# Kernel optimization log

Hardware: AMD Instinct MI355X
Metric: run time of the kernel (lower is better)

## Reference

```python
import jax, jax.numpy as jnp
import numpy as np

B, T, F, C, L, W, NT, H = 4096, 64, 32, 64, 256, 512, 8, 12

# Tsit5 Butcher tableau (fixed-step, 6-stage FSAL-free form)
A21 = 0.161
A31, A32 = -0.008480655492356989, 0.335480655492357
A41, A42, A43 = 2.8971530571054935, -6.359448489975075, 4.362295432869581
A51, A52, A53, A54 = 5.325864828439257, -11.748883564062828, 7.4955393428898365, -0.09249506636175525
A61, A62, A63, A64, A65 = 5.86145544294642, -12.92096931784711, 8.159367898576159, -0.071584973281401, -0.028269050394068383
BC1, BC2, BC3, BC4, BC5, BC6 = 0.09646076681806523, 0.01, 0.4798896504144996, 1.379008574103742, -3.290069515436081, 2.324710524099774
SUBSTEPS = 10  # dt0 = 0.1, integrate each unit interval with 10 fixed steps


def setup_inputs() -> dict:
    key = jax.random.key(0)
    ks = jax.random.split(key, 16)
    def lin(k, out_d, in_d, scale=None):
        s = (1.0 / np.sqrt(in_d)) if scale is None else scale
        return jax.random.normal(k, (out_d, in_d), jnp.float32) * s
    inp = {
        "x_seq": jax.random.normal(ks[0], (B, T, F), jnp.float32),
        "country_idx": jax.random.randint(ks[1], (B,), 0, C),
        "horizon": H,
        # GRU encoder params (equinox GRUCell layout: 3*hidden stacked r,z,n)
        "W_ih": lin(ks[2], 3 * L, F + C),
        "W_hh": lin(ks[3], 3 * L, L),
        "b_ih": jnp.zeros((3 * L,), jnp.float32),
        "b_n": jnp.zeros((L,), jnp.float32),
        # NeuralField MLP 256->512->512->256, small init to keep the ODE stable
        "W0": lin(ks[4], W, L, 0.1 / np.sqrt(L)),
        "b0": jnp.zeros((W,), jnp.float32),
        "W1": lin(ks[5], W, W, 0.1 / np.sqrt(W)),
        "b1": jnp.zeros((W,), jnp.float32),
        "W2": lin(ks[6], L, W, 0.1 / np.sqrt(W)),
        "b2": jnp.zeros((L,), jnp.float32),
        # Decoder
        "W_dec": lin(ks[7], NT, L),
        "b_dec": jnp.zeros((NT,), jnp.float32),
    }
    return inp


def reference(x_seq, W_ih, W_hh, b_ih, b_n, W0, b0, W1, b1, W2, b2, W_dec, b_dec, country_idx, horizon):
    dtype = x_seq.dtype
    n_countries = W_ih.shape[1] - x_seq.shape[2]
    n_latent = W_hh.shape[1]
    ohe = jax.nn.one_hot(country_idx, n_countries, dtype=dtype)  # [B, C]

    # ---- GRU encoder scan over time ----
    h0 = jnp.zeros((x_seq.shape[0], n_latent), dtype)
    def gru_step(h, x_t):
        x_in = jnp.concatenate([x_t, ohe], axis=-1)          # [B, F+C]
        ih = x_in @ W_ih.T + b_ih                            # [B, 3L]
        hh = h @ W_hh.T                                      # [B, 3L]
        ir, iz, inn = jnp.split(ih, 3, axis=-1)
        hr, hz, hn = jnp.split(hh, 3, axis=-1)
        r = jax.nn.sigmoid(ir + hr)
        z = jax.nn.sigmoid(iz + hz)
        n = jnp.tanh(inn + r * (hn + b_n))
        return n + z * (h - n), None
    h_final, _ = jax.lax.scan(gru_step, h0, jnp.swapaxes(x_seq, 0, 1))

    # ---- Neural ODE vector field (autonomous ELU MLP) ----
    def f(y):
        a = jax.nn.elu(y @ W0.T + b0)
        a = jax.nn.elu(a @ W1.T + b1)
        return a @ W2.T + b2

    dt = jnp.asarray(1.0 / SUBSTEPS, dtype)
    def tsit5_step(y, _):
        k1 = f(y)
        k2 = f(y + dt * (A21 * k1))
        k3 = f(y + dt * (A31 * k1 + A32 * k2))
        k4 = f(y + dt * (A41 * k1 + A42 * k2 + A43 * k3))
        k5 = f(y + dt * (A51 * k1 + A52 * k2 + A53 * k3 + A54 * k4))
        k6 = f(y + dt * (A61 * k1 + A62 * k2 + A63 * k3 + A64 * k4 + A65 * k5))
        y_new = y + dt * (BC1 * k1 + BC2 * k2 + BC3 * k3 + BC4 * k4 + BC5 * k5 + BC6 * k6)
        return y_new, None

    def unit(y, _):
        y, _ = jax.lax.scan(tsit5_step, y, None, length=SUBSTEPS)
        return y, y  # save state at each integer time t = 1..horizon

    _, ys = jax.lax.scan(unit, h_final, None, length=horizon)  # [H, B, L]

    # ---- linear decode ----
    out = jnp.einsum('hbl,tl->bht', ys, W_dec) + b_dec  # [B, H, n_targets]
    return out
```

## Files before the change

### kernel.cpp

```cpp
#include <hip/hip_runtime.h>

typedef __bf16 bf16;
typedef __bf16 bf16x8 __attribute__((ext_vector_type(8)));
typedef float  f32x4  __attribute__((ext_vector_type(4)));

#define B_TOT 4096
#define T_SEQ 64
#define NT_OUT 8
#define NTHR 512
#define NBLK 256
#define GSZ  8

#define WS_W0   0
#define WS_W1   262144
#define WS_W2   786432
#define WS_WHH  1048576
#define WS_WIH  1441792
#define WS_BC   1490944
#define WS_GY   2097152
#define WS_GYB  4194304
#define WS_GH1  6291456
#define WS_GH2  10485760
#define WS_FLG  14680064
#define WS_MAP  14688256

constexpr float A21 = 0.161f;
constexpr float A31 = -0.008480655492356989f, A32 = 0.335480655492357f;
constexpr float A41 = 2.8971530571054935f, A42 = -6.359448489975075f, A43 = 4.362295432869581f;
constexpr float A51 = 5.325864828439257f, A52 = -11.748883564062828f, A53 = 7.4955393428898365f, A54 = -0.09249506636175525f;
constexpr float A61 = 5.86145544294642f, A62 = -12.92096931784711f, A63 = 8.159367898576159f, A64 = -0.071584973281401f, A65 = -0.028269050394068383f;
constexpr float BC1 = 0.09646076681806523f, BC2 = 0.01f, BC3 = 0.4798896504144996f;
constexpr float BC4 = 1.379008574103742f, BC5 = -3.290069515436081f, BC6 = 2.324710524099774f;
constexpr float DT = 0.1f;
constexpr float BROW[5][5] = {
    {A21, 0, 0, 0, 0},
    {A31, A32, 0, 0, 0},
    {A41, A42, A43, 0, 0},
    {A51, A52, A53, A54, 0},
    {A61, A62, A63, A64, A65}};
constexpr float FCF[6] = {BC1, BC2, BC3, BC4, BC5, BC6};

__device__ __forceinline__ f32x4 MFMA(bf16x8 a, bf16x8 b, f32x4 c) {
    return __builtin_amdgcn_mfma_f32_16x16x32_bf16(a, b, c, 0, 0, 0);
}
__device__ __forceinline__ float eluf(float x) { return x > 0.f ? x : __expf(x) - 1.f; }
__device__ __forceinline__ float sigm_f(float x) { return 1.f / (1.f + __expf(-x)); }
__device__ __forceinline__ float tanh_f(float x) { return 1.f - 2.f / (__expf(2.f * x) + 1.f); }

template<bool FAST>
__device__ __forceinline__ void ld4g(const bf16* p, bf16x8& a0, bf16x8& a1, bf16x8& a2, bf16x8& a3) {
    if constexpr (FAST) {
        asm volatile(
            "global_load_dwordx4 %0, %4, off sc0\n\t"
            "global_load_dwordx4 %1, %4, off offset:1024 sc0\n\t"
            "global_load_dwordx4 %2, %4, off offset:2048 sc0\n\t"
            "global_load_dwordx4 %3, %4, off offset:3072 sc0"
            : "=&v"(a0), "=&v"(a1), "=&v"(a2), "=&v"(a3)
            : "v"(p) : "memory");
    } else {
        asm volatile(
            "global_load_dwordx4 %0, %4, off sc0 sc1\n\t"
            "global_load_dwordx4 %1, %4, off offset:1024 sc0 sc1\n\t"
            "global_load_dwordx4 %2, %4, off offset:2048 sc0 sc1\n\t"
            "global_load_dwordx4 %3, %4, off offset:3072 sc0 sc1"
            : "=&v"(a0), "=&v"(a1), "=&v"(a2), "=&v"(a3)
            : "v"(p) : "memory");
    }
}
template<bool FAST>
__device__ __forceinline__ bf16x8 ld1g(const bf16* p) {
    bf16x8 a;
    if constexpr (FAST)
        asm volatile("global_load_dwordx4 %0, %1, off sc0\n\ts_waitcnt vmcnt(0)"
                     : "=v"(a) : "v"(p) : "memory");
    else
        asm volatile("global_load_dwordx4 %0, %1, off sc0 sc1\n\ts_waitcnt vmcnt(0)"
                     : "=v"(a) : "v"(p) : "memory");
    return a;
}
template<bool FAST>
__device__ __forceinline__ void st8g(bf16* p, bf16x8 v) {
    if constexpr (FAST) *(bf16x8*)p = v;
    else asm volatile("global_store_dwordx4 %0, %1, off sc0 sc1" :: "v"(p), "v"(v) : "memory");
}
__device__ __forceinline__ void vmwait() {
    asm volatile("s_waitcnt vmcnt(0)" ::: "memory");
    __builtin_amdgcn_sched_barrier(0);
}

__device__ __forceinline__ void produce(unsigned* f, int tid) {
    asm volatile("s_waitcnt vmcnt(0)" ::: "memory");
    __syncthreads();
    if (tid == 0) __hip_atomic_fetch_add(f, 1u, __ATOMIC_RELAXED, __HIP_MEMORY_SCOPE_AGENT);
}
__device__ __forceinline__ void consume(unsigned* f, unsigned tgt, int tid) {
    if (tid == 0) {
        while (__hip_atomic_load(f, __ATOMIC_RELAXED, __HIP_MEMORY_SCOPE_AGENT) < tgt)
            __builtin_amdgcn_s_sleep(8);
    }
    __syncthreads();
}

template<bool FAST>
__device__ __forceinline__ void decode(const bf16* gY, const float* sWdec, const float* sBdec,
                                       float* bncF, float* __restrict__ out,
                                       int tid, int g, int j, int H, int u) {
    {
        const int row = tid >> 5, seg = tid & 31;
        bf16x8 yv = ld1g<FAST>(gY + ((j * 8 + (seg >> 2)) * 64 + row + (seg & 3) * 16) * 8);
        #pragma unroll
        for (int e = 0; e < 8; ++e) bncF[row * 256 + seg * 8 + e] = (float)yv[e];
    }
    __syncthreads();
    if (tid < 128) {
        const int row = tid >> 3, tt = tid & 7;
        float acc = sBdec[tt];
        const float* wd = sWdec + tt * 256;
        const float* yr = bncF + row * 256;
        #pragma unroll 8
        for (int i = 0; i < 256; i += 4) {
            f32x4 yv = *(const f32x4*)&yr[i];
            acc += yv[0] * wd[i] + yv[1] * wd[i + 1] + yv[2] * wd[i + 2] + yv[3] * wd[i + 3];
        }
        out[((size_t)(g * 128 + 16 * j + row) * H + u) * NT_OUT + tt] = acc;
    }
    __syncthreads();
}

template<int ST, bool FAST>
__device__ __forceinline__ void ode_stage(
    const bf16* sW0, const bf16* sW1, const bf16* sW2, bf16* bnc,
    bf16* gY, bf16* gH1, bf16* gH2,
    unsigned* fY, unsigned* fH1, unsigned* fH2,
    const float (&b0r)[4], const float (&b1r)[4], const float (&b2r)[2],
    f32x4 (&yreg)[2], f32x4 (&kreg)[5][2],
    int tid, int m, int lane, int j,
    unsigned& eY, unsigned& eH1, unsigned& eH2) {
    const int lm = lane & 15, q4 = (lane >> 4) << 2;
    const f32x4 Z = {0.f, 0.f, 0.f, 0.f};

    {
        bf16x8 a[8];
        const bf16* pA = gY + m * 4096 + lane * 8;
        ld4g<FAST>(pA, a[0], a[1], a[2], a[3]);
        ld4g<FAST>(pA + 2048, a[4], a[5], a[6], a[7]);
        vmwait();
        f32x4 acc[4] = {Z, Z, Z, Z};
        #pragma unroll
        for (int kk = 0; kk < 8; ++kk)
            #pragma unroll
            for (int nt = 0; nt < 4; ++nt)
                acc[nt] = MFMA(a[kk], *(const bf16x8*)&sW0[(nt * 8 + kk) * 512 + lane * 8], acc[nt]);
        #pragma unroll
        for (int nt = 0; nt < 4; ++nt) {
            const int oct = 2 * (nt & 1) + (lm >> 3);
            const int base = (m * 2 + (nt >> 1)) * 512;
            #pragma unroll
            for (int r = 0; r < 4; ++r)
                bnc[base + ((q4 + r) + oct * 16) * 8 + (lm & 7)] = (bf16)eluf(acc[nt][r] + b0r[nt]);
        }
    }
    __syncthreads();
    {
        const int i = tid * 16, mm = i >> 10, rem = i & 1023;
        bf16* d = gH1 + mm * 8192 + (2 * j + (rem >> 9)) * 512 + (rem & 511);
        st8g<FAST>(d, *(const bf16x8*)&bnc[i]);
        st8g<FAST>(d + 8, *(const bf16x8*)&bnc[i + 8]);
    }
    produce(fH1, tid); ++eH1;
    consume(fH1, GSZ * eH1, tid);

    {
        bf16x8 a[16];
        const bf16* pA = gH1 + m * 8192 + lane * 8;
        ld4g<FAST>(pA, a[0], a[1], a[2], a[3]);
        ld4g<FAST>(pA + 2048, a[4], a[5], a[6], a[7]);
        ld4g<FAST>(pA + 4096, a[8], a[9], a[10], a[11]);
        ld4g<FAST>(pA + 6144, a[12], a[13], a[14], a[15]);
        vmwait();
        f32x4 acc[4] = {Z, Z, Z, Z};
        #pragma unroll
        for (int kk = 0; kk < 16; ++kk)
            #pragma unroll
            for (int nt = 0; nt < 4; ++nt)
                acc[nt] = MFMA(a[kk], *(const bf16x8*)&sW1[(nt * 16 + kk) * 512 + lane * 8], acc[nt]);
        #pragma unroll
        for (int nt = 0; nt < 4; ++nt) {
            const int oct = 2 * (nt & 1) + (lm >> 3);
            const int base = (m * 2 + (nt >> 1)) * 512;
            #pragma unroll
            for (int r = 0; r < 4; ++r)
                bnc[base + ((q4 + r) + oct * 16) * 8 + (lm & 7)] = (bf16)eluf(acc[nt][r] + b1r[nt]);
        }
    }
    __syncthreads();
    {
        const int i = tid * 16, mm = i >> 10, rem = i & 1023;
        bf16* d = gH2 + mm * 8192 + (2 * j + (rem >> 9)) * 512 + (rem & 511);
        st8g<FAST>(d, *(const bf16x8*)&bnc[i]);
        st8g<FAST>(d + 8, *(const bf16x8*)&bnc[i + 8]);
    }
    produce(fH2, tid); ++eH2;
    consume(fH2, GSZ * eH2, tid);

    {
        bf16x8 a[16];
        const bf16* pA = gH2 + m * 8192 + lane * 8;
        ld4g<FAST>(pA, a[0], a[1], a[2], a[3]);
        ld4g<FAST>(pA + 2048, a[4], a[5], a[6], a[7]);
        ld4g<FAST>(pA + 4096, a[8], a[9], a[10], a[11]);
        ld4g<FAST>(pA + 6144, a[12], a[13], a[14], a[15]);
        vmwait();
        f32x4 kk2[2] = {Z, Z};
        #pragma unroll
        for (int kk = 0; kk < 16; ++kk)
            #pragma unroll
            for (int nt = 0; nt < 2; ++nt)
                kk2[nt] = MFMA(a[kk], *(const bf16x8*)&sW2[(nt * 16 + kk) * 512 + lane * 8], kk2[nt]);
        #pragma unroll
        for (int nt = 0; nt < 2; ++nt)
            #pragma unroll
            for (int r = 0; r < 4; ++r) kk2[nt][r] += b2r[nt];

        f32x4 yst[2];
        if constexpr (ST < 5) {
            kreg[ST][0] = kk2[0]; kreg[ST][1] = kk2[1];
            #pragma unroll
            for (int nt = 0; nt < 2; ++nt) {
                yst[nt] = yreg[nt];
                #pragma unroll
                for (int i = 0; i <= ST; ++i) {
                    const float c = DT * BROW[ST][i];
                    #pragma unroll
                    for (int r = 0; r < 4; ++r) yst[nt][r] += c * kreg[i][nt][r];
                }
            }
        } else {
            #pragma unroll
            for (int nt = 0; nt < 2; ++nt) {
                #pragma unroll
                for (int i = 0; i < 5; ++i) {
                    const float c = DT * FCF[i];
                    #pragma unroll
                    for (int r = 0; r < 4; ++r) yreg[nt][r] += c * kreg[i][nt][r];
                }
                #pragma unroll
                for (int r = 0; r < 4; ++r) yreg[nt][r] += (DT * FCF[5]) * kk2[nt][r];
                yst[nt] = yreg[nt];
            }
        }
        #pragma unroll
        for (int nt = 0; nt < 2; ++nt) {
            const int oct = 2 * nt + (lm >> 3);
            #pragma unroll
            for (int r = 0; r < 4; ++r)
                bnc[(m * 64 + (q4 + r) + oct * 16) * 8 + (lm & 7)] = (bf16)yst[nt][r];
        }
    }
    __syncthreads();
    {
        const int i = tid * 8, mm = i >> 9, rem = i & 511;
        st8g<FAST>(gY + mm * 4096 + j * 512 + rem, *(const bf16x8*)&bnc[i]);
    }
    produce(fY, tid); ++eY;
}

template<bool FAST>
__device__ void body(const float* __restrict__ x_seq, const int* __restrict__ cidx,
                     const float* __restrict__ b_n, const float* __restrict__ b0,
                     const float* __restrict__ b1, const float* __restrict__ b2,
                     const float* __restrict__ W_dec, const float* __restrict__ b_dec,
                     char* __restrict__ ws, float* __restrict__ out, char* SM,
                     int H, int g, int j) {
    const int tid = threadIdx.x, m = tid >> 6, lane = tid & 63;
    const int lm = lane & 15, q = lane >> 4, q4 = q << 2;
    const int grow0 = g * 128;

    const bf16* W0p  = (const bf16*)(ws + WS_W0);
    const bf16* W1p  = (const bf16*)(ws + WS_W1);
    const bf16* W2p  = (const bf16*)(ws + WS_W2);
    const bf16* WhhP = (const bf16*)(ws + WS_WHH);
    const bf16* WihP = (const bf16*)(ws + WS_WIH);
    const float* bias_c = (const float*)(ws + WS_BC);
    bf16* gY  = (bf16*)(ws + WS_GY)  + (size_t)g * 32768;
    bf16* gYb = (bf16*)(ws + WS_GYB) + (size_t)g * 32768;
    bf16* gH1 = (bf16*)(ws + WS_GH1) + (size_t)g * 65536;
    bf16* gH2 = (bf16*)(ws + WS_GH2) + (size_t)g * 65536;
    unsigned* fl = (unsigned*)(ws + WS_FLG) + (size_t)g * 64;
    unsigned *fY = fl, *fH1 = fl + 16, *fH2 = fl + 32;

    bf16*  sWgt  = (bf16*)SM;
    bf16*  bnc   = (bf16*)(SM + 131072);
    float* bncF  = (float*)(SM + 131072);
    float* sWdec = (float*)(SM + 147456);
    float* sBdec = (float*)(SM + 155648);

    unsigned eY = 0, eH1 = 0, eH2 = 0;

    for (int i = tid; i < 2048; i += NTHR) sWdec[i] = W_dec[i];
    if (tid < 8) sBdec[tid] = b_dec[tid];

    bf16* sGhh = sWgt;
    bf16* sGih = sWgt + 24576;
    for (int i = tid; i < 3072; i += NTHR) {
        const int gh = i >> 9, inner = (i & 511) << 3;
        const int c = (gh >> 1) * 16 + 2 * j + (gh & 1);
        *(bf16x8*)&sGhh[gh * 4096 + inner] = *(const bf16x8*)&WhhP[(size_t)c * 4096 + inner];
    }
    for (int i = tid; i < 384; i += NTHR) {
        const int gh = i >> 6, inner = (i & 63) << 3;
        const int c = (gh >> 1) * 16 + 2 * j + (gh & 1);
        *(bf16x8*)&sGih[gh * 512 + inner] = *(const bf16x8*)&WihP[(size_t)c * 512 + inner];
    }

    float bcr[2][4], bcz[2][4], bcn[2][4], bnr[2];
    #pragma unroll
    for (int h = 0; h < 2; ++h) {
        const int F = 32 * j + 16 * h + lm;
        bnr[h] = b_n[F];
        #pragma unroll
        for (int r = 0; r < 4; ++r) {
            const int c = cidx[grow0 + 16 * m + q4 + r];
            bcr[h][r] = bias_c[(size_t)c * 768 + F];
            bcz[h][r] = bias_c[(size_t)c * 768 + 256 + F];
            bcn[h][r] = bias_c[(size_t)c * 768 + 512 + F];
        }
    }
    __syncthreads();

    {
        bf16x8 zz;
        #pragma unroll
        for (int e = 0; e < 8; ++e) zz[e] = (bf16)0.f;
        const int i = tid * 8, mm = i >> 9, rem = i & 511;
        st8g<FAST>(gY + mm * 4096 + j * 512 + rem, zz);
    }
    produce(fY, tid); ++eY;

    f32x4 hreg[2] = {{0.f,0.f,0.f,0.f},{0.f,0.f,0.f,0.f}};
    const f32x4 Z = {0.f, 0.f, 0.f, 0.f};

    for (int t = 0; t < T_SEQ; ++t) {
        consume(fY, GSZ * eY, tid);
        const bf16* hb = (t & 1) ? gYb : gY;
        bf16x8 a[8];
        const bf16* pA = hb + m * 4096 + lane * 8;
        ld4g<FAST>(pA, a[0], a[1], a[2], a[3]);
        ld4g<FAST>(pA + 2048, a[4], a[5], a[6], a[7]);
        bf16x8 ax;
        {
            const float* xp = x_seq + (((size_t)(grow0 + 16 * m + lm)) * T_SEQ + t) * 32 + 8 * q;
            f32x4 xa = *(const f32x4*)xp;
            f32x4 xb = *(const f32x4*)(xp + 4);
            #pragma unroll
            for (int e = 0; e < 4; ++e) { ax[e] = (bf16)xa[e]; ax[4 + e] = (bf16)xb[e]; }
        }
        vmwait();
        f32x4 aRZ[4] = {Z, Z, Z, Z}, aNH[2] = {Z, Z}, aNX[2] = {Z, Z};
        #pragma unroll
        for (int kk = 0; kk < 8; ++kk) {
            #pragma unroll
            for (int h = 0; h < 2; ++h) {
                aRZ[h]     = MFMA(a[kk], *(const bf16x8*)&sGhh[(0 + h) * 4096 + kk * 512 + lane * 8], aRZ[h]);
                aRZ[2 + h] = MFMA(a[kk], *(const bf16x8*)&sGhh[(2 + h) * 4096 + kk * 512 + lane * 8], aRZ[2 + h]);
                aNH[h]     = MFMA(a[kk], *(const bf16x8*)&sGhh[(4 + h) * 4096 + kk * 512 + lane * 8], aNH[h]);
            }
        }
        #pragma unroll
        for (int h = 0; h < 2; ++h) {
            aRZ[h]     = MFMA(ax, *(const bf16x8*)&sGih[(0 + h) * 512 + lane * 8], aRZ[h]);
            aRZ[2 + h] = MFMA(ax, *(const bf16x8*)&sGih[(2 + h) * 512 + lane * 8], aRZ[2 + h]);
            aNX[h]     = MFMA(ax, *(const bf16x8*)&sGih[(4 + h) * 512 + lane * 8], aNX[h]);
        }
        #pragma unroll
        for (int h = 0; h < 2; ++h) {
            const int oct = 2 * h + (lm >> 3);
            #pragma unroll
            for (int r = 0; r < 4; ++r) {
                const float rg = sigm_f(aRZ[h][r] + bcr[h][r]);
                const float zg = sigm_f(aRZ[2 + h][r] + bcz[h][r]);
                const float nn = tanh_f(aNX[h][r] + bcn[h][r] + rg * (aNH[h][r] + bnr[h]));
                const float hp = nn + zg * (hreg[h][r] - nn);
                hreg[h][r] = hp;
                bnc[(m * 64 + (q4 + r) + oct * 16) * 8 + (lm & 7)] = (bf16)hp;
            }
        }
        __syncthreads();
        {
            bf16* wb = ((t + 1) & 1) ? gYb : gY;
            const int i = tid * 8, mm = i >> 9, rem = i & 511;
            st8g<FAST>(wb + mm * 4096 + j * 512 + rem, *(const bf16x8*)&bnc[i]);
        }
        produce(fY, tid); ++eY;
    }

    bf16* sW0 = sWgt;
    bf16* sW1 = sWgt + 16384;
    bf16* sW2 = sWgt + 49152;
    for (int i = tid; i < 2048; i += NTHR)
        *(bf16x8*)&sW0[i * 8] = *(const bf16x8*)&W0p[(size_t)j * 16384 + i * 8];
    for (int i = tid; i < 4096; i += NTHR)
        *(bf16x8*)&sW1[i * 8] = *(const bf16x8*)&W1p[(size_t)j * 32768 + i * 8];
    for (int i = tid; i < 2048; i += NTHR)
        *(bf16x8*)&sW2[i * 8] = *(const bf16x8*)&W2p[(size_t)j * 16384 + i * 8];

    float b0r[4], b1r[4], b2r[2];
    #pragma unroll
    for (int nt = 0; nt < 4; ++nt) {
        b0r[nt] = b0[64 * j + nt * 16 + lm];
        b1r[nt] = b1[64 * j + nt * 16 + lm];
    }
    #pragma unroll
    for (int nt = 0; nt < 2; ++nt) b2r[nt] = b2[32 * j + nt * 16 + lm];
    __syncthreads();

    f32x4 yreg[2] = {hreg[0], hreg[1]};
    f32x4 kreg[5][2];

    const int NSS = H * 10;
    for (int ss = 0; ss < NSS; ++ss) {
        consume(fY, GSZ * eY, tid);
        if (ss && (ss % 10) == 0)
            decode<FAST>(gY, sWdec, sBdec, bncF, out, tid, g, j, H, ss / 10 - 1);
        ode_stage<0, FAST>(sW0, sW1, sW2, bnc, gY, gH1, gH2, fY, fH1, fH2, b0r, b1r, b2r, yreg, kreg, tid, m, lane, j, eY, eH1, eH2);
        consume(fY, GSZ * eY, tid);
        ode_stage<1, FAST>(sW0, sW1, sW2, bnc, gY, gH1, gH2, fY, fH1, fH2, b0r, b1r, b2r, yreg, kreg, tid, m, lane, j, eY, eH1, eH2);
        consume(fY, GSZ * eY, tid);
        ode_stage<2, FAST>(sW0, sW1, sW2, bnc, gY, gH1, gH2, fY, fH1, fH2, b0r, b1r, b2r, yreg, kreg, tid, m, lane, j, eY, eH1, eH2);
        consume(fY, GSZ * eY, tid);
        ode_stage<3, FAST>(sW0, sW1, sW2, bnc, gY, gH1, gH2, fY, fH1, fH2, b0r, b1r, b2r, yreg, kreg, tid, m, lane, j, eY, eH1, eH2);
        consume(fY, GSZ * eY, tid);
        ode_stage<4, FAST>(sW0, sW1, sW2, bnc, gY, gH1, gH2, fY, fH1, fH2, b0r, b1r, b2r, yreg, kreg, tid, m, lane, j, eY, eH1, eH2);
        consume(fY, GSZ * eY, tid);
        ode_stage<5, FAST>(sW0, sW1, sW2, bnc, gY, gH1, gH2, fY, fH1, fH2, b0r, b1r, b2r, yreg, kreg, tid, m, lane, j, eY, eH1, eH2);
    }
    consume(fY, GSZ * eY, tid);
    decode<FAST>(gY, sWdec, sBdec, bncF, out, tid, g, j, H, H - 1);
}

__global__ void __launch_bounds__(NTHR, 2)
k_main(const float* __restrict__ x_seq, const int* __restrict__ cidx,
       const float* __restrict__ b_n, const float* __restrict__ b0,
       const float* __restrict__ b1, const float* __restrict__ b2,
       const float* __restrict__ W_dec, const float* __restrict__ b_dec,
       char* __restrict__ ws, float* __restrict__ out, int H) {
    __shared__ __align__(16) char SM[155712];
    const int tid = threadIdx.x, b = blockIdx.x;
    const int x8 = b & 7, rr = b >> 3, mg = rr >> 3, j = rr & 7;
    const int g = x8 * 4 + mg;

    unsigned* xmap = (unsigned*)(ws + WS_MAP);
    unsigned* gctr = (unsigned*)(ws + WS_MAP + 1024);
    unsigned xcc;
    asm volatile("s_getreg_b32 %0, hwreg(HW_REG_XCC_ID)" : "=s"(xcc));
    if (tid == 0) {
        __hip_atomic_store(&xmap[b], xcc, __ATOMIC_RELAXED, __HIP_MEMORY_SCOPE_AGENT);
        __hip_atomic_fetch_add(gctr, 1u, __ATOMIC_RELAXED, __HIP_MEMORY_SCOPE_AGENT);
        while (__hip_atomic_load(gctr, __ATOMIC_RELAXED, __HIP_MEMORY_SCOPE_AGENT) < NBLK)
            __builtin_amdgcn_s_sleep(8);
    }
    __syncthreads();
    unsigned* mapL = (unsigned*)(SM + 131072);
    if (tid < NBLK)
        mapL[tid] = __hip_atomic_load(&xmap[tid], __ATOMIC_RELAXED, __HIP_MEMORY_SCOPE_AGENT);
    __syncthreads();
    int* fastP = (int*)(SM + 155696);
    if (tid == 0) {
        const unsigned my = mapL[b];
        int cnt = 0;
        for (int i = 0; i < NBLK; ++i) cnt += (mapL[i] == my) ? 1 : 0;
        int ok = (cnt == 32) ? 1 : 0;
        for (int i = 0; i < GSZ; ++i) ok &= (mapL[x8 + 8 * (mg * 8 + i)] == my) ? 1 : 0;
        *fastP = ok;
    }
    __syncthreads();
    const int fastf = *fastP;
    __syncthreads();

    if (fastf)
        body<true>(x_seq, cidx, b_n, b0, b1, b2, W_dec, b_dec, ws, out, (char*)SM, H, g, j);
    else
        body<false>(x_seq, cidx, b_n, b0, b1, b2, W_dec, b_dec, ws, out, (char*)SM, H, g, j);
}

__global__ void k_pack(const float* __restrict__ src, bf16* __restrict__ dst,
                       int OUT, int K, int Ksrc, int koff) {
    const int total = (OUT * K) >> 3;
    for (int gg = blockIdx.x * blockDim.x + threadIdx.x; gg < total; gg += gridDim.x * blockDim.x) {
        const int lane = gg & 63, f = gg >> 6;
        const int KK = K >> 5;
        const int kk = f % KK, c = f / KK;
        const int col = c * 16 + (lane & 15);
        const int k0 = kk * 32 + ((lane >> 4) << 3);
        bf16x8 o;
        #pragma unroll
        for (int jj = 0; jj < 8; ++jj) o[jj] = (bf16)src[(size_t)col * Ksrc + koff + k0 + jj];
        *(bf16x8*)&dst[(size_t)gg * 8] = o;
    }
}

__global__ void k_bias(const float* __restrict__ W_ih, const float* __restrict__ b_ih,
                       float* __restrict__ bias_c) {
    const int i = blockIdx.x * blockDim.x + threadIdx.x;
    if (i < 64 * 768) {
        const int c = i / 768, n = i - c * 768;
        bias_c[i] = W_ih[(size_t)n * 96 + 32 + c] + b_ih[n];
    }
}

extern "C" void kernel_launch(void* const* d_in, const int* in_sizes, int n_in,
                              void* d_out, int out_size, void* d_ws, size_t ws_size,
                              hipStream_t stream) {
    const float* x_seq = (const float*)d_in[0];
    const int*   cidx  = (const int*)d_in[1];
    const float* W_ih  = (const float*)d_in[3];
    const float* W_hh  = (const float*)d_in[4];
    const float* b_ih  = (const float*)d_in[5];
    const float* b_n   = (const float*)d_in[6];
    const float* W0    = (const float*)d_in[7];
    const float* b0    = (const float*)d_in[8];
    const float* W1    = (const float*)d_in[9];
    const float* b1    = (const float*)d_in[10];
    const float* W2    = (const float*)d_in[11];
    const float* b2    = (const float*)d_in[12];
    const float* W_dec = (const float*)d_in[13];
    const float* b_dec = (const float*)d_in[14];
    float* out = (float*)d_out;
    const int H = out_size / (B_TOT * NT_OUT);
    char* ws = (char*)d_ws;

    hipMemsetAsync(ws + WS_FLG, 0, 16384, stream);

    k_pack<<<64, 256, 0, stream>>>(W0, (bf16*)(ws + WS_W0), 512, 256, 256, 0);
    k_pack<<<128, 256, 0, stream>>>(W1, (bf16*)(ws + WS_W1), 512, 512, 512, 0);
    k_pack<<<64, 256, 0, stream>>>(W2, (bf16*)(ws + WS_W2), 256, 512, 512, 0);
    k_pack<<<96, 256, 0, stream>>>(W_hh, (bf16*)(ws + WS_WHH), 768, 256, 256, 0);
    k_pack<<<12, 256, 0, stream>>>(W_ih, (bf16*)(ws + WS_WIH), 768, 32, 96, 0);
    k_bias<<<(64 * 768 + 255) / 256, 256, 0, stream>>>(W_ih, b_ih, (float*)(ws + WS_BC));

    k_main<<<NBLK, NTHR, 0, stream>>>(x_seq, cidx, b_n, b0, b1, b2, W_dec, b_dec,
                                      ws, out, H);
}
```

Baseline: 6.731 ms.

## Swap MFMA operands to write outputs directly to global, drop LDS staging

Reorganizes the per-wave GEMM mapping so weights become the A operand and activations the B operand. Each lane can then write its bf16 results straight to the global exchange buffers in the consumer's layout, which removes the LDS bounce buffer and the extra __syncthreads before each store. The decoder is rewritten as a warp-shuffle reduction without LDS staging, GRU weights are interleaved into a single LDS array, and the spin-wait sleep is shortened. The trade-off is smaller, less coalesced 8-byte global stores and changed work partitioning across waves.

```diff
diff --git a/kernel.cpp b/kernel.cpp
--- a/kernel.cpp
+++ b/kernel.cpp
@@ -2,7 +2,9 @@
 
 typedef __bf16 bf16;
 typedef __bf16 bf16x8 __attribute__((ext_vector_type(8)));
+typedef __bf16 bf16x4 __attribute__((ext_vector_type(4)));
 typedef float  f32x4  __attribute__((ext_vector_type(4)));
+typedef unsigned int u32;
 
 #define B_TOT 4096
 #define T_SEQ 64
@@ -17,12 +19,12 @@
 #define WS_WHH  1048576
 #define WS_WIH  1441792
 #define WS_BC   1490944
-#define WS_GY   2097152
-#define WS_GYB  4194304
-#define WS_GH1  6291456
-#define WS_GH2  10485760
-#define WS_FLG  14680064
-#define WS_MAP  14688256
+#define WS_GY   1703936
+#define WS_GYB  3801088
+#define WS_GH1  5898240
+#define WS_GH2  10092544
+#define WS_FLG  14286848
+#define WS_MAP  14290944
 
 constexpr float A21 = 0.161f;
 constexpr float A31 = -0.008480655492356989f, A32 = 0.335480655492357f;
@@ -55,16 +57,14 @@
             "global_load_dwordx4 %1, %4, off offset:1024 sc0\n\t"
             "global_load_dwordx4 %2, %4, off offset:2048 sc0\n\t"
             "global_load_dwordx4 %3, %4, off offset:3072 sc0"
-            : "=&v"(a0), "=&v"(a1), "=&v"(a2), "=&v"(a3)
-            : "v"(p) : "memory");
+            : "=&v"(a0), "=&v"(a1), "=&v"(a2), "=&v"(a3) : "v"(p) : "memory");
     } else {
         asm volatile(
             "global_load_dwordx4 %0, %4, off sc0 sc1\n\t"
             "global_load_dwordx4 %1, %4, off offset:1024 sc0 sc1\n\t"
             "global_load_dwordx4 %2, %4, off offset:2048 sc0 sc1\n\t"
             "global_load_dwordx4 %3, %4, off offset:3072 sc0 sc1"
-            : "=&v"(a0), "=&v"(a1), "=&v"(a2), "=&v"(a3)
-            : "v"(p) : "memory");
+            : "=&v"(a0), "=&v"(a1), "=&v"(a2), "=&v"(a3) : "v"(p) : "memory");
     }
 }
 template<bool FAST>
@@ -79,190 +79,154 @@
     return a;
 }
 template<bool FAST>
-__device__ __forceinline__ void st8g(bf16* p, bf16x8 v) {
-    if constexpr (FAST) *(bf16x8*)p = v;
-    else asm volatile("global_store_dwordx4 %0, %1, off sc0 sc1" :: "v"(p), "v"(v) : "memory");
+__device__ __forceinline__ void st4g(bf16* p, bf16x4 v) {
+    if constexpr (FAST) *(bf16x4*)p = v;
+    else asm volatile("global_store_dwordx2 %0, %1, off sc0 sc1" :: "v"(p), "v"(v) : "memory");
 }
 __device__ __forceinline__ void vmwait() {
     asm volatile("s_waitcnt vmcnt(0)" ::: "memory");
     __builtin_amdgcn_sched_barrier(0);
 }
 
-__device__ __forceinline__ void produce(unsigned* f, int tid) {
+__device__ __forceinline__ void produce(u32* f, int tid) {
     asm volatile("s_waitcnt vmcnt(0)" ::: "memory");
     __syncthreads();
     if (tid == 0) __hip_atomic_fetch_add(f, 1u, __ATOMIC_RELAXED, __HIP_MEMORY_SCOPE_AGENT);
 }
-__device__ __forceinline__ void consume(unsigned* f, unsigned tgt, int tid) {
+__device__ __forceinline__ void consume(const u32* f, u32 tgt, int tid) {
     if (tid == 0) {
         while (__hip_atomic_load(f, __ATOMIC_RELAXED, __HIP_MEMORY_SCOPE_AGENT) < tgt)
-            __builtin_amdgcn_s_sleep(8);
-    }
-    __syncthreads();
-}
-
-template<bool FAST>
-__device__ __forceinline__ void decode(const bf16* gY, const float* sWdec, const float* sBdec,
-                                       float* bncF, float* __restrict__ out,
-                                       int tid, int g, int j, int H, int u) {
-    {
-        const int row = tid >> 5, seg = tid & 31;
-        bf16x8 yv = ld1g<FAST>(gY + ((j * 8 + (seg >> 2)) * 64 + row + (seg & 3) * 16) * 8);
-        #pragma unroll
-        for (int e = 0; e < 8; ++e) bncF[row * 256 + seg * 8 + e] = (float)yv[e];
-    }
-    __syncthreads();
-    if (tid < 128) {
-        const int row = tid >> 3, tt = tid & 7;
-        float acc = sBdec[tt];
-        const float* wd = sWdec + tt * 256;
-        const float* yr = bncF + row * 256;
-        #pragma unroll 8
-        for (int i = 0; i < 256; i += 4) {
-            f32x4 yv = *(const f32x4*)&yr[i];
-            acc += yv[0] * wd[i] + yv[1] * wd[i + 1] + yv[2] * wd[i + 2] + yv[3] * wd[i + 3];
-        }
-        out[((size_t)(g * 128 + 16 * j + row) * H + u) * NT_OUT + tt] = acc;
-    }
-    __syncthreads();
+            __builtin_amdgcn_s_sleep(1);
+    }
+    __syncthreads();
+}
+
+template<int KK, int NM, bool FAST>
+__device__ __forceinline__ void gemm_core(const bf16* sWl, const bf16* ginl, int MSIN,
+                                          f32x4 (&acc)[NM]) {
+    bf16x8 wr[KK];
+    #pragma unroll
+    for (int kk = 0; kk < KK; ++kk) wr[kk] = *(const bf16x8*)&sWl[kk * 512];
+    #pragma unroll
+    for (int m = 0; m < NM; ++m) {
+        bf16x8 a[KK];
+        const bf16* p = ginl + m * MSIN;
+        #pragma unroll
+        for (int kq = 0; kq < KK; kq += 4)
+            ld4g<FAST>(p + kq * 512, a[kq], a[kq + 1], a[kq + 2], a[kq + 3]);
+        vmwait();
+        f32x4 e = {0.f, 0.f, 0.f, 0.f}, o = {0.f, 0.f, 0.f, 0.f};
+        #pragma unroll
+        for (int kk = 0; kk < KK; kk += 2) {
+            e = MFMA(wr[kk], a[kk], e);
+            o = MFMA(wr[kk + 1], a[kk + 1], o);
+        }
+        acc[m] = e + o;
+    }
+}
+
+template<bool ELU, int NM, bool FAST>
+__device__ __forceinline__ void store_out(bf16* dst, int MS, const float (&bias)[4],
+                                          const f32x4 (&acc)[NM]) {
+    #pragma unroll
+    for (int m = 0; m < NM; ++m) {
+        bf16x4 ov;
+        #pragma unroll
+        for (int r = 0; r < 4; ++r) {
+            float v = acc[m][r] + bias[r];
+            if constexpr (ELU) v = eluf(v);
+            ov[r] = (bf16)v;
+        }
+        st4g<FAST>(dst + m * MS, ov);
+    }
 }
 
 template<int ST, bool FAST>
 __device__ __forceinline__ void ode_stage(
-    const bf16* sW0, const bf16* sW1, const bf16* sW2, bf16* bnc,
-    bf16* gY, bf16* gH1, bf16* gH2,
-    unsigned* fY, unsigned* fH1, unsigned* fH2,
-    const float (&b0r)[4], const float (&b1r)[4], const float (&b2r)[2],
+    const bf16* sW0l, const bf16* sW1l, const bf16* sW2l,
+    const bf16* gYl, bf16* gH1d, const bf16* gH1l, bf16* gH2d, const bf16* gH2l, bf16* gYd,
+    u32* fY, u32* fH1, u32* fH2, int tid,
+    const float (&b0w)[4], const float (&b1w)[4], const float (&b2w)[4],
     f32x4 (&yreg)[2], f32x4 (&kreg)[5][2],
-    int tid, int m, int lane, int j,
-    unsigned& eY, unsigned& eH1, unsigned& eH2) {
-    const int lm = lane & 15, q4 = (lane >> 4) << 2;
-    const f32x4 Z = {0.f, 0.f, 0.f, 0.f};
-
+    u32& eY, u32& eH1, u32& eH2) {
     {
-        bf16x8 a[8];
-        const bf16* pA = gY + m * 4096 + lane * 8;
-        ld4g<FAST>(pA, a[0], a[1], a[2], a[3]);
-        ld4g<FAST>(pA + 2048, a[4], a[5], a[6], a[7]);
-        vmwait();
-        f32x4 acc[4] = {Z, Z, Z, Z};
-        #pragma unroll
-        for (int kk = 0; kk < 8; ++kk)
-            #pragma unroll
-            for (int nt = 0; nt < 4; ++nt)
-                acc[nt] = MFMA(a[kk], *(const bf16x8*)&sW0[(nt * 8 + kk) * 512 + lane * 8], acc[nt]);
-        #pragma unroll
-        for (int nt = 0; nt < 4; ++nt) {
-            const int oct = 2 * (nt & 1) + (lm >> 3);
-            const int base = (m * 2 + (nt >> 1)) * 512;
-            #pragma unroll
-            for (int r = 0; r < 4; ++r)
-                bnc[base + ((q4 + r) + oct * 16) * 8 + (lm & 7)] = (bf16)eluf(acc[nt][r] + b0r[nt]);
-        }
-    }
-    __syncthreads();
-    {
-        const int i = tid * 16, mm = i >> 10, rem = i & 1023;
-        bf16* d = gH1 + mm * 8192 + (2 * j + (rem >> 9)) * 512 + (rem & 511);
-        st8g<FAST>(d, *(const bf16x8*)&bnc[i]);
-        st8g<FAST>(d + 8, *(const bf16x8*)&bnc[i + 8]);
+        f32x4 acc[4];
+        gemm_core<8, 4, FAST>(sW0l, gYl, 4096, acc);
+        store_out<true, 4, FAST>(gH1d, 8192, b0w, acc);
     }
     produce(fH1, tid); ++eH1;
     consume(fH1, GSZ * eH1, tid);
-
     {
-        bf16x8 a[16];
-        const bf16* pA = gH1 + m * 8192 + lane * 8;
-        ld4g<FAST>(pA, a[0], a[1], a[2], a[3]);
-        ld4g<FAST>(pA + 2048, a[4], a[5], a[6], a[7]);
-        ld4g<FAST>(pA + 4096, a[8], a[9], a[10], a[11]);
-        ld4g<FAST>(pA + 6144, a[12], a[13], a[14], a[15]);
-        vmwait();
-        f32x4 acc[4] = {Z, Z, Z, Z};
-        #pragma unroll
-        for (int kk = 0; kk < 16; ++kk)
-            #pragma unroll
-            for (int nt = 0; nt < 4; ++nt)
-                acc[nt] = MFMA(a[kk], *(const bf16x8*)&sW1[(nt * 16 + kk) * 512 + lane * 8], acc[nt]);
-        #pragma unroll
-        for (int nt = 0; nt < 4; ++nt) {
-            const int oct = 2 * (nt & 1) + (lm >> 3);
-            const int base = (m * 2 + (nt >> 1)) * 512;
-            #pragma unroll
-            for (int r = 0; r < 4; ++r)
-                bnc[base + ((q4 + r) + oct * 16) * 8 + (lm & 7)] = (bf16)eluf(acc[nt][r] + b1r[nt]);
-        }
-    }
-    __syncthreads();
-    {
-        const int i = tid * 16, mm = i >> 10, rem = i & 1023;
-        bf16* d = gH2 + mm * 8192 + (2 * j + (rem >> 9)) * 512 + (rem & 511);
-        st8g<FAST>(d, *(const bf16x8*)&bnc[i]);
-        st8g<FAST>(d + 8, *(const bf16x8*)&bnc[i + 8]);
+        f32x4 acc[4];
+        gemm_core<16, 4, FAST>(sW1l, gH1l, 8192, acc);
+        store_out<true, 4, FAST>(gH2d, 8192, b1w, acc);
     }
     produce(fH2, tid); ++eH2;
     consume(fH2, GSZ * eH2, tid);
-
     {
-        bf16x8 a[16];
-        const bf16* pA = gH2 + m * 8192 + lane * 8;
-        ld4g<FAST>(pA, a[0], a[1], a[2], a[3]);
-        ld4g<FAST>(pA + 2048, a[4], a[5], a[6], a[7]);
-        ld4g<FAST>(pA + 4096, a[8], a[9], a[10], a[11]);
-        ld4g<FAST>(pA + 6144, a[12], a[13], a[14], a[15]);
-        vmwait();
-        f32x4 kk2[2] = {Z, Z};
-        #pragma unroll
-        for (int kk = 0; kk < 16; ++kk)
+        f32x4 acc[2];
+        gemm_core<16, 2, FAST>(sW2l, gH2l, 8192, acc);
+        #pragma unroll
+        for (int i = 0; i < 2; ++i) {
+            f32x4 kv;
             #pragma unroll
-            for (int nt = 0; nt < 2; ++nt)
-                kk2[nt] = MFMA(a[kk], *(const bf16x8*)&sW2[(nt * 16 + kk) * 512 + lane * 8], kk2[nt]);
-        #pragma unroll
-        for (int nt = 0; nt < 2; ++nt)
-            #pragma unroll
-            for (int r = 0; r < 4; ++r) kk2[nt][r] += b2r[nt];
-
-        f32x4 yst[2];
-        if constexpr (ST < 5) {
-            kreg[ST][0] = kk2[0]; kreg[ST][1] = kk2[1];
-            #pragma unroll
-            for (int nt = 0; nt < 2; ++nt) {
-                yst[nt] = yreg[nt];
+            for (int r = 0; r < 4; ++r) kv[r] = acc[i][r] + b2w[r];
+            f32x4 yst;
+            if constexpr (ST < 5) {
+                kreg[ST][i] = kv;
+                yst = yreg[i];
                 #pragma unroll
-                for (int i = 0; i <= ST; ++i) {
-                    const float c = DT * BROW[ST][i];
+                for (int s = 0; s <= ST; ++s) {
+                    const float c = DT * BROW[ST][s];
                     #pragma unroll
-                    for (int r = 0; r < 4; ++r) yst[nt][r] += c * kreg[i][nt][r];
+                    for (int r = 0; r < 4; ++r) yst[r] += c * kreg[s][i][r];
                 }
-            }
-        } else {
-            #pragma unroll
-            for (int nt = 0; nt < 2; ++nt) {
+            } else {
                 #pragma unroll
-                for (int i = 0; i < 5; ++i) {
-                    const float c = DT * FCF[i];
+                for (int s = 0; s < 5; ++s) {
+                    const float c = DT * FCF[s];
                     #pragma unroll
-                    for (int r = 0; r < 4; ++r) yreg[nt][r] += c * kreg[i][nt][r];
+                    for (int r = 0; r < 4; ++r) yreg[i][r] += c * kreg[s][i][r];
                 }
                 #pragma unroll
-                for (int r = 0; r < 4; ++r) yreg[nt][r] += (DT * FCF[5]) * kk2[nt][r];
-                yst[nt] = yreg[nt];
+                for (int r = 0; r < 4; ++r) yreg[i][r] += (DT * FCF[5]) * kv[r];
+                yst = yreg[i];
             }
-        }
-        #pragma unroll
-        for (int nt = 0; nt < 2; ++nt) {
-            const int oct = 2 * nt + (lm >> 3);
+            bf16x4 ov;
             #pragma unroll
-            for (int r = 0; r < 4; ++r)
-                bnc[(m * 64 + (q4 + r) + oct * 16) * 8 + (lm & 7)] = (bf16)yst[nt][r];
-        }
-    }
-    __syncthreads();
-    {
-        const int i = tid * 8, mm = i >> 9, rem = i & 511;
-        st8g<FAST>(gY + mm * 4096 + j * 512 + rem, *(const bf16x8*)&bnc[i]);
+            for (int r = 0; r < 4; ++r) ov[r] = (bf16)yst[r];
+            st4g<FAST>(gYd + i * 4096, ov);
+        }
     }
     produce(fY, tid); ++eY;
+}
+
+template<bool FAST>
+__device__ __forceinline__ void dec_unit(const bf16* gY, const float* sWdec, const float* sBdec,
+                                         float* out, int g, int j, int w, int lane, int H, int u) {
+    const int rloc = 2 * w + (lane >> 5);
+    const int li = lane & 31;
+    const bf16* p = gY + (size_t)j * 4096 + (((li >> 2) * 64 + (li & 3) * 16 + rloc)) * 8;
+    bf16x8 yv = ld1g<FAST>(p);
+    const int f0 = li * 8;
+    float acc[8];
+    #pragma unroll
+    for (int t = 0; t < 8; ++t) acc[t] = 0.f;
+    #pragma unroll
+    for (int e = 0; e < 8; ++e) {
+        const float yf = (float)yv[e];
+        #pragma unroll
+        for (int t = 0; t < 8; ++t) acc[t] += yf * sWdec[t * 256 + f0 + e];
+    }
+    #pragma unroll
+    for (int k = 1; k < 32; k <<= 1)
+        #pragma unroll
+        for (int t = 0; t < 8; ++t) acc[t] += __shfl_xor(acc[t], k, 64);
+    if (li == 0) {
+        const size_t row = (size_t)g * 128 + 16 * j + rloc;
+        #pragma unroll
+        for (int t = 0; t < 8; ++t) out[(row * H + u) * NT_OUT + t] = acc[t] + sBdec[t];
+    }
 }
 
 template<bool FAST>
@@ -272,7 +236,7 @@
                      const float* __restrict__ W_dec, const float* __restrict__ b_dec,
                      char* __restrict__ ws, float* __restrict__ out, char* SM,
                      int H, int g, int j) {
-    const int tid = threadIdx.x, m = tid >> 6, lane = tid & 63;
+    const int tid = threadIdx.x, w = tid >> 6, lane = tid & 63;
     const int lm = lane & 15, q = lane >> 4, q4 = q << 2;
     const int grow0 = g * 128;
 
@@ -286,110 +250,103 @@
     bf16* gYb = (bf16*)(ws + WS_GYB) + (size_t)g * 32768;
     bf16* gH1 = (bf16*)(ws + WS_GH1) + (size_t)g * 65536;
     bf16* gH2 = (bf16*)(ws + WS_GH2) + (size_t)g * 65536;
-    unsigned* fl = (unsigned*)(ws + WS_FLG) + (size_t)g * 64;
-    unsigned *fY = fl, *fH1 = fl + 16, *fH2 = fl + 32;
+    u32* fl  = (u32*)(ws + WS_FLG + (size_t)g * 128);
+    u32 *fY = fl, *fH1 = fl + 16, *fH2 = fl + 32;
 
     bf16*  sWgt  = (bf16*)SM;
-    bf16*  bnc   = (bf16*)(SM + 131072);
-    float* bncF  = (float*)(SM + 131072);
-    float* sWdec = (float*)(SM + 147456);
+    float* sWdec = (float*)(SM + 131072);
+    float* yx    = (float*)(SM + 139264);
     float* sBdec = (float*)(SM + 155648);
 
-    unsigned eY = 0, eH1 = 0, eH2 = 0;
+    u32 eY = 0, eH1 = 0, eH2 = 0;
 
     for (int i = tid; i < 2048; i += NTHR) sWdec[i] = W_dec[i];
     if (tid < 8) sBdec[tid] = b_dec[tid];
-
-    bf16* sGhh = sWgt;
-    bf16* sGih = sWgt + 24576;
-    for (int i = tid; i < 3072; i += NTHR) {
-        const int gh = i >> 9, inner = (i & 511) << 3;
-        const int c = (gh >> 1) * 16 + 2 * j + (gh & 1);
-        *(bf16x8*)&sGhh[gh * 4096 + inner] = *(const bf16x8*)&WhhP[(size_t)c * 4096 + inner];
-    }
-    for (int i = tid; i < 384; i += NTHR) {
-        const int gh = i >> 6, inner = (i & 63) << 3;
-        const int c = (gh >> 1) * 16 + 2 * j + (gh & 1);
-        *(bf16x8*)&sGih[gh * 512 + inner] = *(const bf16x8*)&WihP[(size_t)c * 512 + inner];
-    }
-
-    float bcr[2][4], bcz[2][4], bcn[2][4], bnr[2];
-    #pragma unroll
-    for (int h = 0; h < 2; ++h) {
-        const int F = 32 * j + 16 * h + lm;
-        bnr[h] = b_n[F];
-        #pragma unroll
-        for (int r = 0; r < 4; ++r) {
-            const int c = cidx[grow0 + 16 * m + q4 + r];
-            bcr[h][r] = bias_c[(size_t)c * 768 + F];
-            bcz[h][r] = bias_c[(size_t)c * 768 + 256 + F];
-            bcn[h][r] = bias_c[(size_t)c * 768 + 512 + F];
-        }
-    }
-    __syncthreads();
-
+    for (int i = tid; i < 54 * 64; i += NTHR) {
+        const int fr = i >> 6, l = i & 63;
+        const int tau = fr / 9, kk = fr % 9;
+        const int gam = tau >> 1, p = tau & 1;
+        const int c = gam * 16 + 2 * j + p;
+        const bf16* src = (kk < 8) ? &WhhP[(((size_t)c) * 8 + kk) * 512 + l * 8]
+                                   : &WihP[((size_t)c) * 512 + l * 8];
+        *(bf16x8*)&sWgt[((size_t)fr) * 512 + l * 8] = *(const bf16x8*)src;
+    }
+
+    const int m = w;
+    float bcr[2][4], bcz[2][4], bcn[2][4], bnr[2][4];
     {
-        bf16x8 zz;
-        #pragma unroll
-        for (int e = 0; e < 8; ++e) zz[e] = (bf16)0.f;
-        const int i = tid * 8, mm = i >> 9, rem = i & 511;
-        st8g<FAST>(gY + mm * 4096 + j * 512 + rem, zz);
+        const int c = cidx[grow0 + 16 * m + lm];
+        #pragma unroll
+        for (int p = 0; p < 2; ++p)
+            #pragma unroll
+            for (int r = 0; r < 4; ++r) {
+                const int F = 32 * j + p * 16 + q4 + r;
+                bcr[p][r] = bias_c[(size_t)c * 768 + F];
+                bcz[p][r] = bias_c[(size_t)c * 768 + 256 + F];
+                bcn[p][r] = bias_c[(size_t)c * 768 + 512 + F];
+                bnr[p][r] = b_n[F];
+            }
+    }
+    int dgru[2];
+    #pragma unroll
+    for (int p = 0; p < 2; ++p)
+        dgru[p] = (j * 64 + ((4 * j + 2 * p + (q >> 1)) & 3) * 16 + lm) * 8 + (q & 1) * 4;
+
+    {
+        bf16x4 z4;
+        #pragma unroll
+        for (int r = 0; r < 4; ++r) z4[r] = (bf16)0.f;
+        st4g<FAST>(gY + m * 4096 + dgru[0], z4);
+        st4g<FAST>(gY + m * 4096 + dgru[1], z4);
     }
     produce(fY, tid); ++eY;
 
-    f32x4 hreg[2] = {{0.f,0.f,0.f,0.f},{0.f,0.f,0.f,0.f}};
+    f32x4 hreg[2] = {{0.f, 0.f, 0.f, 0.f}, {0.f, 0.f, 0.f, 0.f}};
     const f32x4 Z = {0.f, 0.f, 0.f, 0.f};
-
     for (int t = 0; t < T_SEQ; ++t) {
-        consume(fY, GSZ * eY, tid);
-        const bf16* hb = (t & 1) ? gYb : gY;
-        bf16x8 a[8];
-        const bf16* pA = hb + m * 4096 + lane * 8;
-        ld4g<FAST>(pA, a[0], a[1], a[2], a[3]);
-        ld4g<FAST>(pA + 2048, a[4], a[5], a[6], a[7]);
         bf16x8 ax;
         {
-            const float* xp = x_seq + (((size_t)(grow0 + 16 * m + lm)) * T_SEQ + t) * 32 + 8 * q;
+            const float* xp = x_seq + (((size_t)(grow0 + 16 * m + lm)) * T_SEQ + t) * 32 + q * 8;
             f32x4 xa = *(const f32x4*)xp;
             f32x4 xb = *(const f32x4*)(xp + 4);
             #pragma unroll
             for (int e = 0; e < 4; ++e) { ax[e] = (bf16)xa[e]; ax[4 + e] = (bf16)xb[e]; }
         }
+        consume(fY, GSZ * eY, tid);
+        const bf16* hs = ((t & 1) ? gYb : gY) + m * 4096 + lane * 8;
+        bf16x8 a[8];
+        ld4g<FAST>(hs, a[0], a[1], a[2], a[3]);
+        ld4g<FAST>(hs + 2048, a[4], a[5], a[6], a[7]);
         vmwait();
-        f32x4 aRZ[4] = {Z, Z, Z, Z}, aNH[2] = {Z, Z}, aNX[2] = {Z, Z};
+        f32x4 rz[4] = {Z, Z, Z, Z}, nH[2] = {Z, Z}, nX[2] = {Z, Z};
         #pragma unroll
         for (int kk = 0; kk < 8; ++kk) {
             #pragma unroll
-            for (int h = 0; h < 2; ++h) {
-                aRZ[h]     = MFMA(a[kk], *(const bf16x8*)&sGhh[(0 + h) * 4096 + kk * 512 + lane * 8], aRZ[h]);
-                aRZ[2 + h] = MFMA(a[kk], *(const bf16x8*)&sGhh[(2 + h) * 4096 + kk * 512 + lane * 8], aRZ[2 + h]);
-                aNH[h]     = MFMA(a[kk], *(const bf16x8*)&sGhh[(4 + h) * 4096 + kk * 512 + lane * 8], aNH[h]);
+            for (int p = 0; p < 2; ++p) {
+                rz[p]     = MFMA(*(const bf16x8*)&sWgt[((0 + p) * 9 + kk) * 512 + lane * 8], a[kk], rz[p]);
+                rz[2 + p] = MFMA(*(const bf16x8*)&sWgt[((2 + p) * 9 + kk) * 512 + lane * 8], a[kk], rz[2 + p]);
+                nH[p]     = MFMA(*(const bf16x8*)&sWgt[((4 + p) * 9 + kk) * 512 + lane * 8], a[kk], nH[p]);
             }
         }
         #pragma unroll
-        for (int h = 0; h < 2; ++h) {
-            aRZ[h]     = MFMA(ax, *(const bf16x8*)&sGih[(0 + h) * 512 + lane * 8], aRZ[h]);
-            aRZ[2 + h] = MFMA(ax, *(const bf16x8*)&sGih[(2 + h) * 512 + lane * 8], aRZ[2 + h]);
-            aNX[h]     = MFMA(ax, *(const bf16x8*)&sGih[(4 + h) * 512 + lane * 8], aNX[h]);
-        }
-        #pragma unroll
-        for (int h = 0; h < 2; ++h) {
-            const int oct = 2 * h + (lm >> 3);
+        for (int p = 0; p < 2; ++p) {
+            rz[p]     = MFMA(*(const bf16x8*)&sWgt[((0 + p) * 9 + 8) * 512 + lane * 8], ax, rz[p]);
+            rz[2 + p] = MFMA(*(const bf16x8*)&sWgt[((2 + p) * 9 + 8) * 512 + lane * 8], ax, rz[2 + p]);
+            nX[p]     = MFMA(*(const bf16x8*)&sWgt[((4 + p) * 9 + 8) * 512 + lane * 8], ax, nX[p]);
+        }
+        bf16* hd = (((t + 1) & 1) ? gYb : gY) + m * 4096;
+        #pragma unroll
+        for (int p = 0; p < 2; ++p) {
+            bf16x4 ov;
             #pragma unroll
             for (int r = 0; r < 4; ++r) {
-                const float rg = sigm_f(aRZ[h][r] + bcr[h][r]);
-                const float zg = sigm_f(aRZ[2 + h][r] + bcz[h][r]);
-                const float nn = tanh_f(aNX[h][r] + bcn[h][r] + rg * (aNH[h][r] + bnr[h]));
-                const float hp = nn + zg * (hreg[h][r] - nn);
-                hreg[h][r] = hp;
-                bnc[(m * 64 + (q4 + r) + oct * 16) * 8 + (lm & 7)] = (bf16)hp;
+                const float rg = sigm_f(rz[p][r] + bcr[p][r]);
+                const float zg = sigm_f(rz[2 + p][r] + bcz[p][r]);
+                const float nn = tanh_f(nX[p][r] + bcn[p][r] + rg * (nH[p][r] + bnr[p][r]));
+                hreg[p][r] = nn + zg * (hreg[p][r] - nn);
+                ov[r] = (bf16)hreg[p][r];
             }
-        }
-        __syncthreads();
-        {
-            bf16* wb = ((t + 1) & 1) ? gYb : gY;
-            const int i = tid * 8, mm = i >> 9, rem = i & 511;
-            st8g<FAST>(wb + mm * 4096 + j * 512 + rem, *(const bf16x8*)&bnc[i]);
+            st4g<FAST>(hd + dgru[p], ov);
         }
         produce(fY, tid); ++eY;
     }
@@ -403,39 +360,67 @@
         *(bf16x8*)&sW1[i * 8] = *(const bf16x8*)&W1p[(size_t)j * 32768 + i * 8];
     for (int i = tid; i < 2048; i += NTHR)
         *(bf16x8*)&sW2[i * 8] = *(const bf16x8*)&W2p[(size_t)j * 16384 + i * 8];
-
-    float b0r[4], b1r[4], b2r[2];
-    #pragma unroll
-    for (int nt = 0; nt < 4; ++nt) {
-        b0r[nt] = b0[64 * j + nt * 16 + lm];
-        b1r[nt] = b1[64 * j + nt * 16 + lm];
-    }
-    #pragma unroll
-    for (int nt = 0; nt < 2; ++nt) b2r[nt] = b2[32 * j + nt * 16 + lm];
-    __syncthreads();
-
-    f32x4 yreg[2] = {hreg[0], hreg[1]};
-    f32x4 kreg[5][2];
+    #pragma unroll
+    for (int p = 0; p < 2; ++p)
+        #pragma unroll
+        for (int r = 0; r < 4; ++r)
+            yx[((m * 32) + p * 16 + q4 + r) * 16 + lm] = hreg[p][r];
+    __syncthreads();
+
+    const int nt01 = w >> 1, mh = w & 1, mb01 = mh * 4;
+    const int nt2 = w >> 2, mq = w & 3, mb2 = mq * 2;
+
+    float b0w[4], b1w[4], b2w[4];
+    #pragma unroll
+    for (int r = 0; r < 4; ++r) {
+        b0w[r] = b0[64 * j + nt01 * 16 + q4 + r];
+        b1w[r] = b1[64 * j + nt01 * 16 + q4 + r];
+        b2w[r] = b2[32 * j + nt2 * 16 + q4 + r];
+    }
+    f32x4 yreg[2], kreg[5][2];
+    #pragma unroll
+    for (int i = 0; i < 2; ++i)
+        #pragma unroll
+        for (int r = 0; r < 4; ++r)
+            yreg[i][r] = yx[((mb2 + i) * 32 + nt2 * 16 + q4 + r) * 16 + lm];
+
+    const bf16* sW0l = sW0 + nt01 * 8 * 512 + lane * 8;
+    const bf16* sW1l = sW1 + nt01 * 16 * 512 + lane * 8;
+    const bf16* sW2l = sW2 + nt2 * 16 * 512 + lane * 8;
+    const bf16* gYl  = gY + mb01 * 4096 + lane * 8;
+    const bf16* gH1l = gH1 + mb01 * 8192 + lane * 8;
+    const bf16* gH2l = gH2 + mb2 * 8192 + lane * 8;
+    const int d01 = ((2 * j + (nt01 >> 1)) * 64 + ((8 * j + 2 * nt01 + (q >> 1)) & 3) * 16 + lm) * 8 + (q & 1) * 4;
+    const int d2  = (j * 64 + ((4 * j + 2 * nt2 + (q >> 1)) & 3) * 16 + lm) * 8 + (q & 1) * 4;
+    bf16* gH1d = gH1 + mb01 * 8192 + d01;
+    bf16* gH2d = gH2 + mb01 * 8192 + d01;
+    bf16* gYd  = gY + mb2 * 4096 + d2;
 
     const int NSS = H * 10;
     for (int ss = 0; ss < NSS; ++ss) {
         consume(fY, GSZ * eY, tid);
-        if (ss && (ss % 10) == 0)
-            decode<FAST>(gY, sWdec, sBdec, bncF, out, tid, g, j, H, ss / 10 - 1);
-        ode_stage<0, FAST>(sW0, sW1, sW2, bnc, gY, gH1, gH2, fY, fH1, fH2, b0r, b1r, b2r, yreg, kreg, tid, m, lane, j, eY, eH1, eH2);
-        consume(fY, GSZ * eY, tid);
-        ode_stage<1, FAST>(sW0, sW1, sW2, bnc, gY, gH1, gH2, fY, fH1, fH2, b0r, b1r, b2r, yreg, kreg, tid, m, lane, j, eY, eH1, eH2);
-        consume(fY, GSZ * eY, tid);
-        ode_stage<2, FAST>(sW0, sW1, sW2, bnc, gY, gH1, gH2, fY, fH1, fH2, b0r, b1r, b2r, yreg, kreg, tid, m, lane, j, eY, eH1, eH2);
-        consume(fY, GSZ * eY, tid);
-        ode_stage<3, FAST>(sW0, sW1, sW2, bnc, gY, gH1, gH2, fY, fH1, fH2, b0r, b1r, b2r, yreg, kreg, tid, m, lane, j, eY, eH1, eH2);
-        consume(fY, GSZ * eY, tid);
-        ode_stage<4, FAST>(sW0, sW1, sW2, bnc, gY, gH1, gH2, fY, fH1, fH2, b0r, b1r, b2r, yreg, kreg, tid, m, lane, j, eY, eH1, eH2);
-        consume(fY, GSZ * eY, tid);
-        ode_stage<5, FAST>(sW0, sW1, sW2, bnc, gY, gH1, gH2, fY, fH1, fH2, b0r, b1r, b2r, yreg, kreg, tid, m, lane, j, eY, eH1, eH2);
+        if (ss && ss % 10 == 0)
+            dec_unit<FAST>(gY, sWdec, sBdec, out, g, j, w, lane, H, ss / 10 - 1);
+        ode_stage<0, FAST>(sW0l, sW1l, sW2l, gYl, gH1d, gH1l, gH2d, gH2l, gYd,
+                           fY, fH1, fH2, tid, b0w, b1w, b2w, yreg, kreg, eY, eH1, eH2);
+        consume(fY, GSZ * eY, tid);
+        ode_stage<1, FAST>(sW0l, sW1l, sW2l, gYl, gH1d, gH1l, gH2d, gH2l, gYd,
+                           fY, fH1, fH2, tid, b0w, b1w, b2w, yreg, kreg, eY, eH1, eH2);
+        consume(fY, GSZ * eY, tid);
+        ode_stage<2, FAST>(sW0l, sW1l, sW2l, gYl, gH1d, gH1l, gH2d, gH2l, gYd,
+                           fY, fH1, fH2, tid, b0w, b1w, b2w, yreg, kreg, eY, eH1, eH2);
+        consume(fY, GSZ * eY, tid);
+        ode_stage<3, FAST>(sW0l, sW1l, sW2l, gYl, gH1d, gH1l, gH2d, gH2l, gYd,
+                           fY, fH1, fH2, tid, b0w, b1w, b2w, yreg, kreg, eY, eH1, eH2);
+        consume(fY, GSZ * eY, tid);
+        ode_stage<4, FAST>(sW0l, sW1l, sW2l, gYl, gH1d, gH1l, gH2d, gH2l, gYd,
+                           fY, fH1, fH2, tid, b0w, b1w, b2w, yreg, kreg, eY, eH1, eH2);
+        consume(fY, GSZ * eY, tid);
+        ode_stage<5, FAST>(sW0l, sW1l, sW2l, gYl, gH1d, gH1l, gH2d, gH2l, gYd,
+                           fY, fH1, fH2, tid, b0w, b1w, b2w, yreg, kreg, eY, eH1, eH2);
     }
     consume(fY, GSZ * eY, tid);
-    decode<FAST>(gY, sWdec, sBdec, bncF, out, tid, g, j, H, H - 1);
+    dec_unit<FAST>(gY, sWdec, sBdec, out, g, j, w, lane, H, H - 1);
 }
 
 __global__ void __launch_bounds__(NTHR, 2)
@@ -449,9 +434,9 @@
     const int x8 = b & 7, rr = b >> 3, mg = rr >> 3, j = rr & 7;
     const int g = x8 * 4 + mg;
 
-    unsigned* xmap = (unsigned*)(ws + WS_MAP);
-    unsigned* gctr = (unsigned*)(ws + WS_MAP + 1024);
-    unsigned xcc;
+    u32* xmap = (u32*)(ws + WS_MAP);
+    u32* gctr = (u32*)(ws + WS_MAP + 1024);
+    u32 xcc;
     asm volatile("s_getreg_b32 %0, hwreg(HW_REG_XCC_ID)" : "=s"(xcc));
     if (tid == 0) {
         __hip_atomic_store(&xmap[b], xcc, __ATOMIC_RELAXED, __HIP_MEMORY_SCOPE_AGENT);
@@ -460,13 +445,13 @@
             __builtin_amdgcn_s_sleep(8);
     }
     __syncthreads();
-    unsigned* mapL = (unsigned*)(SM + 131072);
+    u32* mapL = (u32*)(SM + 139264);
     if (tid < NBLK)
         mapL[tid] = __hip_atomic_load(&xmap[tid], __ATOMIC_RELAXED, __HIP_MEMORY_SCOPE_AGENT);
     __syncthreads();
-    int* fastP = (int*)(SM + 155696);
+    int* fastP = (int*)(SM + 155680);
     if (tid == 0) {
-        const unsigned my = mapL[b];
+        const u32 my = mapL[b];
         int cnt = 0;
         for (int i = 0; i < NBLK; ++i) cnt += (mapL[i] == my) ? 1 : 0;
         int ok = (cnt == 32) ? 1 : 0;
@@ -529,7 +514,7 @@
     const int H = out_size / (B_TOT * NT_OUT);
     char* ws = (char*)d_ws;
 
-    hipMemsetAsync(ws + WS_FLG, 0, 16384, stream);
+    hipMemsetAsync(ws + WS_FLG, 0, 8192, stream);
 
     k_pack<<<64, 256, 0, stream>>>(W0, (bf16*)(ws + WS_W0), 512, 256, 256, 0);
     k_pack<<<128, 256, 0, stream>>>(W1, (bf16*)(ws + WS_W1), 512, 512, 512, 0);
```

After: 12.03 ms. +78.8%, slower.
